# Kernel optimization log

Measured on AMD Instinct MI355X. Metric: run time of the kernel, lower is better.

## Reference

```python
import jax, jax.numpy as jnp
import numpy as np

HEAD = 2

def setup_inputs() -> dict:
    key = jax.random.key(0)
    ks = jax.random.split(key, 12)
    B, C, H, W = 4, 512, 64, 64
    IC = 256
    N = H * W
    s = 0.02
    return {
        "x": jax.random.normal(ks[0], (B, C, H, W), jnp.float32),
        "output_attn": jax.random.normal(ks[1], (B, C, H, W), jnp.float32),
        "mlp_w": jax.random.normal(ks[2], (N, N), jnp.float32) * s,
        "mlp_b": jax.random.normal(ks[3], (N,), jnp.float32) * s,
        "g_w": jax.random.normal(ks[4], (IC, C), jnp.float32) * s,
        "g_b": jax.random.normal(ks[5], (IC,), jnp.float32) * s,
        "theta_w": jax.random.normal(ks[6], (IC, C), jnp.float32) * s,
        "theta_b": jax.random.normal(ks[7], (IC,), jnp.float32) * s,
        "phi_w": jax.random.normal(ks[8], (IC, C), jnp.float32) * s,
        "phi_b": jax.random.normal(ks[9], (IC,), jnp.float32) * s,
        "out_w": jax.random.normal(ks[10], (C, IC), jnp.float32) * s,
        "out_b": jax.random.normal(ks[11], (C,), jnp.float32) * s,
    }

def _conv1x1(feat, w, b):
    # feat: [B, Cin, N], w: [Cout, Cin], b: [Cout] -> [B, Cout, N]
    return jnp.einsum('bcn,oc->bon', feat, w) + b[None, :, None]

def reference(x, output_attn, mlp_w, mlp_b, g_w, g_b, theta_w, theta_b,
              phi_w, phi_b, out_w, out_b):
    B, C, H, W = x.shape
    N = H * W
    IC = g_w.shape[0]
    d = IC // HEAD  # per-head dim

    xf = x.reshape(B, C, N)
    # head-MLP remix: only hd==HEAD slice is non-empty (integer-division bug in source)
    xf = xf + (jnp.einsum('bcn,mn->bcm', xf, mlp_w) + mlp_b)

    g = _conv1x1(xf, g_w, g_b)                       # [B, IC, N]
    g = g.reshape(B * HEAD, d, N).transpose(0, 2, 1)  # [BH, N, d]

    oa = output_attn.reshape(B, C, N)
    th = _conv1x1(oa, theta_w, theta_b).reshape(B * HEAD, d, N).transpose(0, 2, 1)  # [BH, N, d]
    ph = _conv1x1(xf, phi_w, phi_b).reshape(B * HEAD, d, N)                          # [BH, d, N]

    scale = 1.0 / (d ** 0.5)
    attn = jax.nn.softmax(jnp.einsum('bnd,bdm->bnm', th, ph) * scale, axis=-1)  # [BH, N, N]
    y = jnp.einsum('bnm,bmd->bnd', attn, g)           # [BH, N, d]
    y = y.reshape(B, HEAD, N, d).transpose(0, 2, 1, 3).reshape(B, N, IC)
    y = y.transpose(0, 2, 1)                          # [B, IC, N]

    out = output_attn + _conv1x1(y, out_w, out_b).reshape(B, C, H, W)
    return out
```

## Files before the change

kernel.cpp:

```cpp
#include <hip/hip_runtime.h>

typedef unsigned short us;
typedef us s8v __attribute__((ext_vector_type(8)));
typedef us s4v __attribute__((ext_vector_type(4)));
typedef float f4v __attribute__((ext_vector_type(4)));
typedef float f16v __attribute__((ext_vector_type(16)));
typedef __bf16 b2v __attribute__((ext_vector_type(2)));

static __device__ __forceinline__ us f2b(float f) {
  return __builtin_bit_cast(us, (__bf16)f);
}
static __device__ __forceinline__ unsigned f2b2(float lo, float hi) {
  b2v v = {(__bf16)lo, (__bf16)hi};
  return __builtin_bit_cast(unsigned, v);
}
static __device__ __forceinline__ float b2f(us s) {
  unsigned u = ((unsigned)s) << 16;
  return __builtin_bit_cast(float, u);
}

#define GLDS(src, dst)                                                        \
  __builtin_amdgcn_global_load_lds(                                           \
      (const __attribute__((address_space(1))) unsigned int*)(src),           \
      (__attribute__((address_space(3))) unsigned int*)(dst), 16, 0, 0)

__global__ __launch_bounds__(256) void castk(const float* __restrict__ in,
                                             us* __restrict__ out, int n4) {
  int i = blockIdx.x * 256 + threadIdx.x;
  int stride = gridDim.x * 256;
  for (; i < n4; i += stride) {
    float4 v = ((const float4*)in)[i];
    s4v s = {f2b(v.x), f2b(v.y), f2b(v.z), f2b(v.w)};
    ((s4v*)out)[i] = s;
  }
}

__global__ __launch_bounds__(256) void wcast4(const float* __restrict__ s0, us* __restrict__ o0,
                                              const float* __restrict__ s1, us* __restrict__ o1,
                                              const float* __restrict__ s2, us* __restrict__ o2,
                                              const float* __restrict__ s3, us* __restrict__ o3) {
  const float* s; us* o;
  int y = blockIdx.y;
  if (y == 0) { s = s0; o = o0; }
  else if (y == 1) { s = s1; o = o1; }
  else if (y == 2) { s = s2; o = o2; }
  else { s = s3; o = o3; }
  int i = blockIdx.x * 256 + threadIdx.x;
  for (; i < 32768; i += 8192) {
    float4 v = ((const float4*)s)[i];
    s4v r = {f2b(v.x), f2b(v.y), f2b(v.z), f2b(v.w)};
    ((s4v*)o)[i] = r;
  }
}

__global__ __launch_bounds__(256) void tcast(const float* __restrict__ in,
                                             us* __restrict__ out, int R, int C,
                                             us* __restrict__ out2) {
  __shared__ float t[64][65];
  const int tid = threadIdx.x;
  const long r0 = (long)blockIdx.y * 64, c0 = (long)blockIdx.x * 64;
#pragma unroll
  for (int j = 0; j < 4; ++j) {
    int idx = j * 256 + tid;
    int row = idx >> 4, c4 = (idx & 15) * 4;
    float4 v = *(const float4*)(in + (r0 + row) * C + c0 + c4);
    t[row][c4] = v.x; t[row][c4 + 1] = v.y; t[row][c4 + 2] = v.z; t[row][c4 + 3] = v.w;
    if (out2) {
      s4v s = {f2b(v.x), f2b(v.y), f2b(v.z), f2b(v.w)};
      *(s4v*)(out2 + (r0 + row) * C + c0 + c4) = s;
    }
  }
  __syncthreads();
#pragma unroll
  for (int j = 0; j < 4; ++j) {
    int idx = j * 256 + tid;
    int orow = idx >> 4, r4 = (idx & 15) * 4;
    s4v s = {f2b(t[r4][orow]), f2b(t[r4 + 1][orow]), f2b(t[r4 + 2][orow]), f2b(t[r4 + 3][orow])};
    *(s4v*)(out + (c0 + orow) * R + r0 + r4) = s;
  }
}

#define SW(row, kb) ((row) * 128 + ((kb) ^ (((row) & 7) << 4)))

template <int EPI, int AF32, int BF32, int SWZ>
__global__ __launch_bounds__(256) void gemm_nt(
    const void* __restrict__ Av, const void* __restrict__ Bv,
    int lda, int ldb, int K, long aZ, long bZ,
    const float* __restrict__ bias,
    const us* __restrict__ addb16,
    const float* __restrict__ addf32,
    us* __restrict__ outb16,
    float* __restrict__ outf32) {
  __shared__ __align__(16) us lA2[2][128 * 64];
  __shared__ __align__(16) us lB2[2][128 * 64];
  const int tid = threadIdx.x, l = tid & 63;
  const int lr = l & 15, lg = l >> 4;
  const int w = tid >> 6, wr = w >> 1, wc = w & 1;
  int bm, bn;
  if constexpr (SWZ) {
    int flat = blockIdx.y * gridDim.x + blockIdx.x;
    int re = (flat & 7) * ((gridDim.x * gridDim.y) >> 3) + (flat >> 3);
    bm = re % gridDim.x; bn = re / gridDim.x;
  } else { bm = blockIdx.x; bn = blockIdx.y; }
  const int z = blockIdx.z;
  const f4v zero = {0.f, 0.f, 0.f, 0.f};
  f4v acc[4][4];
#pragma unroll
  for (int i = 0; i < 4; ++i)
#pragma unroll
    for (int j = 0; j < 4; ++j) acc[i][j] = zero;

  int rS[4], cS[4];
#pragma unroll
  for (int j = 0; j < 4; ++j) {
    int byte = j * 4096 + tid * 16;
    rS[j] = byte >> 7;
    cS[j] = (byte & 127) ^ ((rS[j] & 7) << 4);
  }
  const char* Ab = (const char*)Av + ((long)z * aZ + (long)bm * 128 * lda) * 2;
  const char* Bb = (const char*)Bv + ((long)z * bZ + (long)bn * 128 * ldb) * 2;

  auto stage = [&](int bufi, int k0) {
    char* lab = (char*)lA2[bufi];
    char* lbb = (char*)lB2[bufi];
#pragma unroll
    for (int j = 0; j < 4; ++j) {
      if constexpr (AF32) {
        int byte = j * 4096 + tid * 16;
        int row = byte >> 7, kb = byte & 127;
        const float* af = (const float*)Av + (long)z * aZ + (long)(bm * 128 + row) * lda + k0 + (kb >> 1);
        float4 v0 = *(const float4*)af, v1 = *(const float4*)(af + 4);
        s8v va = {f2b(v0.x), f2b(v0.y), f2b(v0.z), f2b(v0.w), f2b(v1.x), f2b(v1.y), f2b(v1.z), f2b(v1.w)};
        *(s8v*)(lab + SW(row, kb)) = va;
      } else {
        GLDS(Ab + (long)rS[j] * lda * 2 + k0 * 2 + cS[j], lab + j * 4096 + w * 1024);
      }
      if constexpr (BF32) {
        int byte = j * 4096 + tid * 16;
        int row = byte >> 7, kb = byte & 127;
        const float* bf_ = (const float*)Bv + (long)z * bZ + (long)(bn * 128 + row) * ldb + k0 + (kb >> 1);
        float4 v0 = *(const float4*)bf_, v1 = *(const float4*)(bf_ + 4);
        s8v vb = {f2b(v0.x), f2b(v0.y), f2b(v0.z), f2b(v0.w), f2b(v1.x), f2b(v1.y), f2b(v1.z), f2b(v1.w)};
        *(s8v*)(lbb + SW(row, kb)) = vb;
      } else {
        GLDS(Bb + (long)rS[j] * ldb * 2 + k0 * 2 + cS[j], lbb + j * 4096 + w * 1024);
      }
    }
  };

  stage(0, 0);
  for (int k0 = 0; k0 < K; k0 += 64) {
    const int cur = (k0 >> 6) & 1;
    __syncthreads();
    if (k0 + 64 < K) stage(cur ^ 1, k0 + 64);
    const char* lab = (const char*)lA2[cur];
    const char* lbb = (const char*)lB2[cur];
#pragma unroll
    for (int ks = 0; ks < 2; ++ks) {
      s8v af[4], bf[4];
      const int kb = ks * 64 + lg * 16;
#pragma unroll
      for (int mi = 0; mi < 4; ++mi) {
        int row = wr * 64 + mi * 16 + lr;
        af[mi] = *(const s8v*)(lab + SW(row, kb));
      }
#pragma unroll
      for (int ni = 0; ni < 4; ++ni) {
        int row = wc * 64 + ni * 16 + lr;
        bf[ni] = *(const s8v*)(lbb + SW(row, kb));
      }
#pragma unroll
      for (int mi = 0; mi < 4; ++mi)
#pragma unroll
        for (int ni = 0; ni < 4; ++ni)
          acc[mi][ni] = __builtin_amdgcn_mfma_f32_16x16x32_bf16(af[mi], bf[ni], acc[mi][ni], 0, 0, 0);
    }
  }

#pragma unroll
  for (int mi = 0; mi < 4; ++mi) {
#pragma unroll
    for (int ni = 0; ni < 4; ++ni) {
#pragma unroll
      for (int r = 0; r < 4; ++r) {
        int row = bm * 128 + wr * 64 + mi * 16 + lg * 4 + r;
        int col = bn * 128 + wc * 64 + ni * 16 + lr;
        float v = acc[mi][ni][r];
        if constexpr (EPI == 0) {
          long idx = (long)row * 2048 + col;
          outb16[idx] = f2b(v + b2f(addb16[idx]) + bias[row]);
        } else if constexpr (EPI == 1) {
          long idx = ((long)(z * 2 + (col >> 7)) * 4096 + row) * 128 + (col & 127);
          outb16[idx] = f2b(v + bias[col]);
        } else if constexpr (EPI == 2) {
          long idx = ((long)(z * 256 + row)) * 4096 + col;
          outb16[idx] = f2b(v + bias[row]);
        } else {
          long idx = ((long)(z * 512 + row)) * 4096 + col;
          outf32[idx] = v + bias[row] + addf32[idx];
        }
      }
    }
  }
}

__global__ __launch_bounds__(256, 2) void attn_k(const us* __restrict__ th,
                                                 const us* __restrict__ pht,
                                                 const us* __restrict__ g,
                                                 us* __restrict__ pY,
                                                 float2* __restrict__ pml) {
  __shared__ __align__(16) us ph2[2][64 * 128];
  __shared__ __align__(16) us g2[2][128 * 64];
  const int tid = threadIdx.x, l = tid & 63, w = tid >> 6;
  const int l31 = l & 31, h = l >> 5;
  const int swz = (l & 7) << 4;
  const int flat = blockIdx.y * 32 + blockIdx.x;
  const int bh = flat & 7, rest = flat >> 3;
  const int half = rest & 1, qb = rest >> 1;
  const int b = bh >> 1, head = bh & 1;
  const int m00 = half * 2048;
  const float C1 = 0.12751802f;
  const f16v zero16 = {0.f};

  const char* phsrc = (const char*)(pht + (long)bh * 4096 * 128);
  const char* gsrc = (const char*)(g + (long)(b * 256 + head * 128) * 4096);

  int koff[4], voff[4];
#pragma unroll
  for (int j = 0; j < 4; ++j) {
    int d = j * 4096 + tid * 16;
    koff[j] = d ^ (((d >> 8) & 7) << 4);
    int rowg = d >> 7, kbg = d & 127;
    voff[j] = rowg * 8192 + (kbg ^ ((rowg & 7) << 4));
  }

  s8v qf[8];
  {
    const us* thp = th + ((long)bh * 4096 + qb * 128 + w * 32 + l31) * 128 + h * 8;
#pragma unroll
    for (int ks = 0; ks < 8; ++ks) qf[ks] = *(const s8v*)(thp + ks * 16);
  }

  f16v acc0 = zero16, acc1 = zero16, acc2 = zero16, acc3 = zero16;
  float m_run = -1e30f, l_run = 0.f;

  auto stage = [&](int bufi, int m0) {
    char* dk = (char*)ph2[bufi] + w * 1024;
    char* dv = (char*)g2[bufi] + w * 1024;
    const char* sk = phsrc + (long)m0 * 256;
    const char* sv = gsrc + (long)m0 * 2;
#pragma unroll
    for (int j = 0; j < 4; ++j) {
      GLDS(sk + koff[j], dk + j * 4096);
      GLDS(sv + voff[j], dv + j * 4096);
    }
  };

  stage(0, m00);
  __syncthreads();

  for (int t = 0; t < 32; ++t) {
    const int cur = t & 1;
    stage(cur ^ 1, m00 + ((t + 1) & 31) * 64);
    const char* phb = (const char*)ph2[cur];
    const char* gb = (const char*)g2[cur];

    f16v sA[2] = {zero16, zero16};
    __builtin_amdgcn_s_setprio(1);
#pragma unroll
    for (int ks = 0; ks < 8; ++ks) {
#pragma unroll
      for (int mt = 0; mt < 2; ++mt) {
        s8v kf = *(const s8v*)(phb + (mt * 32 + l31) * 256 + (((ks * 32) + h * 16) ^ swz));
        sA[mt] = __builtin_amdgcn_mfma_f32_32x32x16_bf16(kf, qf[ks], sA[mt], 0, 0, 0);
      }
    }
    __builtin_amdgcn_s_setprio(0);

    float mx = sA[0][0];
#pragma unroll
    for (int r = 1; r < 16; ++r) mx = fmaxf(mx, sA[0][r]);
#pragma unroll
    for (int r = 0; r < 16; ++r) mx = fmaxf(mx, sA[1][r]);
    mx = fmaxf(mx, __shfl_xor(mx, 32, 64));

    if (__any(mx > m_run + 60.0f)) {
      float mn = fmaxf(m_run, mx);
      float corr = __builtin_amdgcn_exp2f((m_run - mn) * C1);
      m_run = mn;
      l_run *= corr;
#pragma unroll
      for (int r = 0; r < 16; ++r) {
        acc0[r] *= corr; acc1[r] *= corr; acc2[r] *= corr; acc3[r] *= corr;
      }
    }

    const float nm = -m_run * C1;
    float sum = 0.f;
    s8v bfrag[4];
#pragma unroll
    for (int mt = 0; mt < 2; ++mt) {
#pragma unroll
      for (int k1 = 0; k1 < 2; ++k1) {
        const int base = k1 * 8;
        float p0 = __builtin_amdgcn_exp2f(__builtin_fmaf(sA[mt][base + 0], C1, nm));
        float p1 = __builtin_amdgcn_exp2f(__builtin_fmaf(sA[mt][base + 1], C1, nm));
        float p2 = __builtin_amdgcn_exp2f(__builtin_fmaf(sA[mt][base + 2], C1, nm));
        float p3 = __builtin_amdgcn_exp2f(__builtin_fmaf(sA[mt][base + 3], C1, nm));
        float p4 = __builtin_amdgcn_exp2f(__builtin_fmaf(sA[mt][base + 4], C1, nm));
        float p5 = __builtin_amdgcn_exp2f(__builtin_fmaf(sA[mt][base + 5], C1, nm));
        float p6 = __builtin_amdgcn_exp2f(__builtin_fmaf(sA[mt][base + 6], C1, nm));
        float p7 = __builtin_amdgcn_exp2f(__builtin_fmaf(sA[mt][base + 7], C1, nm));
        sum += ((p0 + p1) + (p2 + p3)) + ((p4 + p5) + (p6 + p7));
        unsigned E0 = f2b2(p0, p1), E1 = f2b2(p2, p3);
        unsigned O0 = f2b2(p4, p5), O1 = f2b2(p6, p7);
        asm("v_permlane32_swap_b32 %0, %1" : "+v"(E0), "+v"(O0));
        asm("v_permlane32_swap_b32 %0, %1" : "+v"(E1), "+v"(O1));
        uint4 u = {E0, E1, O0, O1};
        bfrag[mt * 2 + k1] = __builtin_bit_cast(s8v, u);
      }
    }
    sum += __shfl_xor(sum, 32, 64);
    l_run += sum;

    __builtin_amdgcn_s_setprio(1);
#pragma unroll
    for (int ks2 = 0; ks2 < 4; ++ks2) {
      const int kb = ((ks2 * 32) + h * 16) ^ swz;
      s8v v0 = *(const s8v*)(gb + (l31) * 128 + kb);
      s8v v1 = *(const s8v*)(gb + (32 + l31) * 128 + kb);
      s8v v2 = *(const s8v*)(gb + (64 + l31) * 128 + kb);
      s8v v3 = *(const s8v*)(gb + (96 + l31) * 128 + kb);
      acc0 = __builtin_amdgcn_mfma_f32_32x32x16_bf16(v0, bfrag[ks2], acc0, 0, 0, 0);
      acc1 = __builtin_amdgcn_mfma_f32_32x32x16_bf16(v1, bfrag[ks2], acc1, 0, 0, 0);
      acc2 = __builtin_amdgcn_mfma_f32_32x32x16_bf16(v2, bfrag[ks2], acc2, 0, 0, 0);
      acc3 = __builtin_amdgcn_mfma_f32_32x32x16_bf16(v3, bfrag[ks2], acc3, 0, 0, 0);
    }
    __builtin_amdgcn_s_setprio(0);

    __syncthreads();
  }

  const long gq = (long)bh * 4096 + qb * 128 + w * 32 + l31;
  if (h == 0) pml[gq * 2 + half] = make_float2(m_run, l_run);
  us* py = pY + (gq * 2 + half) * 128;
#pragma unroll
  for (int gi = 0; gi < 4; ++gi) {
    int r0 = gi * 4;
    {
      uint2 u = {f2b2(acc0[r0], acc0[r0 + 1]), f2b2(acc0[r0 + 2], acc0[r0 + 3])};
      *(uint2*)(py + gi * 8 + 4 * h) = u;
    }
    {
      uint2 u = {f2b2(acc1[r0], acc1[r0 + 1]), f2b2(acc1[r0 + 2], acc1[r0 + 3])};
      *(uint2*)(py + 32 + gi * 8 + 4 * h) = u;
    }
    {
      uint2 u = {f2b2(acc2[r0], acc2[r0 + 1]), f2b2(acc2[r0 + 2], acc2[r0 + 3])};
      *(uint2*)(py + 64 + gi * 8 + 4 * h) = u;
    }
    {
      uint2 u = {f2b2(acc3[r0], acc3[r0 + 1]), f2b2(acc3[r0 + 2], acc3[r0 + 3])};
      *(uint2*)(py + 96 + gi * 8 + 4 * h) = u;
    }
  }
}

__global__ __launch_bounds__(256) void mergek(const us* __restrict__ pY,
                                              const float2* __restrict__ pml,
                                              us* __restrict__ yt) {
  const float C1 = 0.12751802f;
  int idx = blockIdx.x * 256 + threadIdx.x;
  int gq = idx >> 4, dd8 = (idx & 15) * 8;
  float2 A = pml[gq * 2 + 0], B = pml[gq * 2 + 1];
  float M = fmaxf(A.x, B.x);
  float e0 = __builtin_amdgcn_exp2f((A.x - M) * C1);
  float e1 = __builtin_amdgcn_exp2f((B.x - M) * C1);
  float inv = 1.0f / (A.y * e0 + B.y * e1);
  e0 *= inv; e1 *= inv;
  s8v Y0 = *(const s8v*)(pY + ((long)gq * 2 + 0) * 128 + dd8);
  s8v Y1 = *(const s8v*)(pY + ((long)gq * 2 + 1) * 128 + dd8);
  s8v o;
#pragma unroll
  for (int i = 0; i < 8; ++i) o[i] = f2b(e0 * b2f(Y0[i]) + e1 * b2f(Y1[i]));
  int bh = gq >> 12, q = gq & 4095, b = bh >> 1, head = bh & 1;
  *(s8v*)(yt + ((long)b * 4096 + q) * 256 + head * 128 + dd8) = o;
}

extern "C" void kernel_launch(void* const* d_in, const int* in_sizes, int n_in,
                              void* d_out, int out_size, void* d_ws, size_t ws_size,
                              hipStream_t stream) {
  (void)in_sizes; (void)n_in; (void)out_size;
  const float* x       = (const float*)d_in[0];
  const float* oa      = (const float*)d_in[1];
  const float* mlp_w   = (const float*)d_in[2];
  const float* mlp_b   = (const float*)d_in[3];
  const float* g_w     = (const float*)d_in[4];
  const float* g_b     = (const float*)d_in[5];
  const float* theta_w = (const float*)d_in[6];
  const float* theta_b = (const float*)d_in[7];
  const float* phi_w   = (const float*)d_in[8];
  const float* phi_b   = (const float*)d_in[9];
  const float* out_w   = (const float*)d_in[10];
  const float* out_b   = (const float*)d_in[11];
  float* out = (float*)d_out;
  char* ws = (char*)d_ws;

  us* xf_t   = (us*)(ws + 0L);
  us* pY     = (us*)(ws + 0L);
  us* oat    = (us*)(ws + 16777216L);
  float2* pml = (float2*)(ws + 16777216L);
  us* xt     = (us*)(ws + 33554432L);
  us* g_ws   = (us*)(ws + 33554432L);
  us* th_ws  = (us*)(ws + 41943040L);
  us* xc     = (us*)(ws + 50331648L);
  us* ph_ws  = (us*)(ws + 50331648L);
  us* yt     = (us*)(ws + 58720256L);
  us* g_wb   = (us*)(ws + 67108864L);
  us* th_wb  = (us*)(ws + 67371008L);
  us* ph_wb  = (us*)(ws + 67633152L);
  us* out_wb = (us*)(ws + 67895296L);
  us* mlp_wb = (us*)(ws + 68157440L);
  const bool big = ws_size >= 101711872ULL;

  wcast4<<<dim3(32, 4), dim3(256), 0, stream>>>(g_w, g_wb, theta_w, th_wb,
                                                phi_w, ph_wb, out_w, out_wb);
  tcast<<<dim3(64, 32), dim3(256), 0, stream>>>(x, xt, 2048, 4096, xc);
  tcast<<<dim3(64, 32), dim3(256), 0, stream>>>(oa, oat, 2048, 4096, nullptr);

  if (big) {
    castk<<<dim3(1024), dim3(256), 0, stream>>>(mlp_w, mlp_wb, 4194304);
    gemm_nt<0, 0, 0, 1><<<dim3(32, 16, 1), dim3(256), 0, stream>>>(
        mlp_wb, xc, 4096, 4096, 4096, 0, 0, mlp_b, xt, nullptr, xf_t, nullptr);
  } else {
    gemm_nt<0, 1, 0, 1><<<dim3(32, 16, 1), dim3(256), 0, stream>>>(
        mlp_w, xc, 4096, 4096, 4096, 0, 0, mlp_b, xt, nullptr, xf_t, nullptr);
  }

  gemm_nt<1, 0, 0, 0><<<dim3(32, 2, 4), dim3(256), 0, stream>>>(
      oat, th_wb, 2048, 512, 512, 512, 0, theta_b, nullptr, nullptr, th_ws, nullptr);
  gemm_nt<1, 0, 0, 0><<<dim3(32, 2, 4), dim3(256), 0, stream>>>(
      xf_t, ph_wb, 2048, 512, 512, 512, 0, phi_b, nullptr, nullptr, ph_ws, nullptr);
  gemm_nt<2, 0, 0, 0><<<dim3(2, 32, 4), dim3(256), 0, stream>>>(
      g_wb, xf_t, 512, 2048, 512, 0, 512, g_b, nullptr, nullptr, g_ws, nullptr);

  attn_k<<<dim3(32, 16), dim3(256), 0, stream>>>(th_ws, ph_ws, g_ws, pY, pml);
  mergek<<<dim3(2048), dim3(256), 0, stream>>>(pY, pml, yt);

  gemm_nt<3, 0, 0, 0><<<dim3(4, 32, 4), dim3(256), 0, stream>>>(
      out_wb, yt, 256, 256, 256, 0, 1048576L, out_b, nullptr, oa, nullptr, out);
}
```

Measured before the change: 255.5 us.

## Use triple-buffered half-K tiles with explicit vmcnt waits in gemm and attention

Both the GEMM and attention kernels move from double-buffered 64-wide K tiles to triple-buffered 32-wide tiles, prefetching two stages ahead. A partial s_waitcnt vmcnt(4) plus a raw barrier replaces __syncthreads, so the next tile's loads can stay in flight while the current one is computed. The GEMM drops its LDS swizzle, which may bring back bank conflicts. The attention kernel halves per-iteration work, doubling loop count and barriers, and issues fewer MFMAs between syncs.

```diff
diff --git a/kernel.cpp b/kernel.cpp
--- a/kernel.cpp
+++ b/kernel.cpp
@@ -23,6 +23,13 @@
   __builtin_amdgcn_global_load_lds(                                           \
       (const __attribute__((address_space(1))) unsigned int*)(src),           \
       (__attribute__((address_space(3))) unsigned int*)(dst), 16, 0, 0)
+
+#define WAITBAR_VM4()  do { asm volatile("s_waitcnt vmcnt(4)" ::: "memory");  \
+  __builtin_amdgcn_sched_barrier(0); __builtin_amdgcn_s_barrier(); } while (0)
+#define WAITBAR_VM0()  do { asm volatile("s_waitcnt vmcnt(0)" ::: "memory");  \
+  __builtin_amdgcn_sched_barrier(0); __builtin_amdgcn_s_barrier(); } while (0)
+#define WAITBAR_ALL()  do { asm volatile("s_waitcnt vmcnt(0) lgkmcnt(0)" ::: "memory"); \
+  __builtin_amdgcn_sched_barrier(0); __builtin_amdgcn_s_barrier(); } while (0)
 
 __global__ __launch_bounds__(256) void castk(const float* __restrict__ in,
                                              us* __restrict__ out, int n4) {
@@ -80,8 +87,6 @@
   }
 }
 
-#define SW(row, kb) ((row) * 128 + ((kb) ^ (((row) & 7) << 4)))
-
 template <int EPI, int AF32, int BF32, int SWZ>
 __global__ __launch_bounds__(256) void gemm_nt(
     const void* __restrict__ Av, const void* __restrict__ Bv,
@@ -91,8 +96,8 @@
     const float* __restrict__ addf32,
     us* __restrict__ outb16,
     float* __restrict__ outf32) {
-  __shared__ __align__(16) us lA2[2][128 * 64];
-  __shared__ __align__(16) us lB2[2][128 * 64];
+  __shared__ __align__(16) us lA[3][128 * 32];
+  __shared__ __align__(16) us lB[3][128 * 32];
   const int tid = threadIdx.x, l = tid & 63;
   const int lr = l & 15, lg = l >> 4;
   const int w = tid >> 6, wr = w >> 1, wc = w & 1;
@@ -110,71 +115,60 @@
 #pragma unroll
     for (int j = 0; j < 4; ++j) acc[i][j] = zero;
 
-  int rS[4], cS[4];
-#pragma unroll
-  for (int j = 0; j < 4; ++j) {
-    int byte = j * 4096 + tid * 16;
-    rS[j] = byte >> 7;
-    cS[j] = (byte & 127) ^ ((rS[j] & 7) << 4);
-  }
   const char* Ab = (const char*)Av + ((long)z * aZ + (long)bm * 128 * lda) * 2;
   const char* Bb = (const char*)Bv + ((long)z * bZ + (long)bn * 128 * ldb) * 2;
 
   auto stage = [&](int bufi, int k0) {
-    char* lab = (char*)lA2[bufi];
-    char* lbb = (char*)lB2[bufi];
-#pragma unroll
-    for (int j = 0; j < 4; ++j) {
+#pragma unroll
+    for (int j = 0; j < 2; ++j) {
+      const int d = j * 4096 + tid * 16;
+      const int row = d >> 6, kb = d & 63;
       if constexpr (AF32) {
-        int byte = j * 4096 + tid * 16;
-        int row = byte >> 7, kb = byte & 127;
         const float* af = (const float*)Av + (long)z * aZ + (long)(bm * 128 + row) * lda + k0 + (kb >> 1);
         float4 v0 = *(const float4*)af, v1 = *(const float4*)(af + 4);
         s8v va = {f2b(v0.x), f2b(v0.y), f2b(v0.z), f2b(v0.w), f2b(v1.x), f2b(v1.y), f2b(v1.z), f2b(v1.w)};
-        *(s8v*)(lab + SW(row, kb)) = va;
+        *(s8v*)((char*)lA[bufi] + d) = va;
       } else {
-        GLDS(Ab + (long)rS[j] * lda * 2 + k0 * 2 + cS[j], lab + j * 4096 + w * 1024);
+        GLDS(Ab + (long)row * lda * 2 + k0 * 2 + kb, (char*)lA[bufi] + j * 4096 + w * 1024);
       }
       if constexpr (BF32) {
-        int byte = j * 4096 + tid * 16;
-        int row = byte >> 7, kb = byte & 127;
         const float* bf_ = (const float*)Bv + (long)z * bZ + (long)(bn * 128 + row) * ldb + k0 + (kb >> 1);
         float4 v0 = *(const float4*)bf_, v1 = *(const float4*)(bf_ + 4);
         s8v vb = {f2b(v0.x), f2b(v0.y), f2b(v0.z), f2b(v0.w), f2b(v1.x), f2b(v1.y), f2b(v1.z), f2b(v1.w)};
-        *(s8v*)(lbb + SW(row, kb)) = vb;
+        *(s8v*)((char*)lB[bufi] + d) = vb;
       } else {
-        GLDS(Bb + (long)rS[j] * ldb * 2 + k0 * 2 + cS[j], lbb + j * 4096 + w * 1024);
+        GLDS(Bb + (long)row * ldb * 2 + k0 * 2 + kb, (char*)lB[bufi] + j * 4096 + w * 1024);
       }
     }
   };
 
+  const int NT = K >> 5;
   stage(0, 0);
-  for (int k0 = 0; k0 < K; k0 += 64) {
-    const int cur = (k0 >> 6) & 1;
-    __syncthreads();
-    if (k0 + 64 < K) stage(cur ^ 1, k0 + 64);
-    const char* lab = (const char*)lA2[cur];
-    const char* lbb = (const char*)lB2[cur];
-#pragma unroll
-    for (int ks = 0; ks < 2; ++ks) {
-      s8v af[4], bf[4];
-      const int kb = ks * 64 + lg * 16;
-#pragma unroll
-      for (int mi = 0; mi < 4; ++mi) {
-        int row = wr * 64 + mi * 16 + lr;
-        af[mi] = *(const s8v*)(lab + SW(row, kb));
-      }
-#pragma unroll
-      for (int ni = 0; ni < 4; ++ni) {
-        int row = wc * 64 + ni * 16 + lr;
-        bf[ni] = *(const s8v*)(lbb + SW(row, kb));
-      }
-#pragma unroll
-      for (int mi = 0; mi < 4; ++mi)
-#pragma unroll
-        for (int ni = 0; ni < 4; ++ni)
-          acc[mi][ni] = __builtin_amdgcn_mfma_f32_16x16x32_bf16(af[mi], bf[ni], acc[mi][ni], 0, 0, 0);
-    }
+  stage(1, 32);
+  if constexpr (AF32 || BF32) { WAITBAR_ALL(); } else { WAITBAR_VM4(); }
+
+  for (int t = 0; t < NT; ++t) {
+    const int cur = t % 3;
+    const bool more = (t + 2 < NT);
+    if (more) stage((t + 2) % 3, (t + 2) * 32);
+    const char* lab = (const char*)lA[cur];
+    const char* lbb = (const char*)lB[cur];
+    s8v af[4], bf[4];
+#pragma unroll
+    for (int mi = 0; mi < 4; ++mi)
+      af[mi] = *(const s8v*)(lab + (wr * 64 + mi * 16 + lr) * 64 + lg * 16);
+#pragma unroll
+    for (int ni = 0; ni < 4; ++ni)
+      bf[ni] = *(const s8v*)(lbb + (wc * 64 + ni * 16 + lr) * 64 + lg * 16);
+    __builtin_amdgcn_s_setprio(1);
+#pragma unroll
+    for (int mi = 0; mi < 4; ++mi)
+#pragma unroll
+      for (int ni = 0; ni < 4; ++ni)
+        acc[mi][ni] = __builtin_amdgcn_mfma_f32_16x16x32_bf16(af[mi], bf[ni], acc[mi][ni], 0, 0, 0);
+    __builtin_amdgcn_s_setprio(0);
+    if constexpr (AF32 || BF32) { WAITBAR_ALL(); }
+    else if (more) { WAITBAR_VM4(); } else { WAITBAR_VM0(); }
   }
 
 #pragma unroll
@@ -209,11 +203,10 @@
                                                  const us* __restrict__ g,
                                                  us* __restrict__ pY,
                                                  float2* __restrict__ pml) {
-  __shared__ __align__(16) us ph2[2][64 * 128];
-  __shared__ __align__(16) us g2[2][128 * 64];
+  __shared__ __align__(16) us ph3[3][32 * 128];
+  __shared__ __align__(16) us g3[3][128 * 32];
   const int tid = threadIdx.x, l = tid & 63, w = tid >> 6;
   const int l31 = l & 31, h = l >> 5;
-  const int swz = (l & 7) << 4;
   const int flat = blockIdx.y * 32 + blockIdx.x;
   const int bh = flat & 7, rest = flat >> 3;
   const int half = rest & 1, qb = rest >> 1;
@@ -225,15 +218,6 @@
   const char* phsrc = (const char*)(pht + (long)bh * 4096 * 128);
   const char* gsrc = (const char*)(g + (long)(b * 256 + head * 128) * 4096);
 
-  int koff[4], voff[4];
-#pragma unroll
-  for (int j = 0; j < 4; ++j) {
-    int d = j * 4096 + tid * 16;
-    koff[j] = d ^ (((d >> 8) & 7) << 4);
-    int rowg = d >> 7, kbg = d & 127;
-    voff[j] = rowg * 8192 + (kbg ^ ((rowg & 7) << 4));
-  }
-
   s8v qf[8];
   {
     const us* thp = th + ((long)bh * 4096 + qb * 128 + w * 32 + l31) * 128 + h * 8;
@@ -245,43 +229,39 @@
   float m_run = -1e30f, l_run = 0.f;
 
   auto stage = [&](int bufi, int m0) {
-    char* dk = (char*)ph2[bufi] + w * 1024;
-    char* dv = (char*)g2[bufi] + w * 1024;
-    const char* sk = phsrc + (long)m0 * 256;
-    const char* sv = gsrc + (long)m0 * 2;
-#pragma unroll
-    for (int j = 0; j < 4; ++j) {
-      GLDS(sk + koff[j], dk + j * 4096);
-      GLDS(sv + voff[j], dv + j * 4096);
+#pragma unroll
+    for (int j = 0; j < 2; ++j) {
+      const int d = j * 4096 + tid * 16;
+      const int rk = d >> 8, kk = (d & 255) ^ ((rk & 7) << 4);
+      GLDS(phsrc + (long)(m0 + rk) * 256 + kk, (char*)ph3[bufi] + j * 4096 + w * 1024);
+      const int rv = d >> 6, kv = (d & 63) ^ ((rv & 3) << 4);
+      GLDS(gsrc + (long)rv * 8192 + m0 * 2 + kv, (char*)g3[bufi] + j * 4096 + w * 1024);
     }
   };
 
   stage(0, m00);
-  __syncthreads();
-
-  for (int t = 0; t < 32; ++t) {
-    const int cur = t & 1;
-    stage(cur ^ 1, m00 + ((t + 1) & 31) * 64);
-    const char* phb = (const char*)ph2[cur];
-    const char* gb = (const char*)g2[cur];
-
-    f16v sA[2] = {zero16, zero16};
+  stage(1, m00 + 32);
+  WAITBAR_VM4();
+
+  for (int t = 0; t < 64; ++t) {
+    const int cur = t % 3;
+    const bool more = (t + 2 < 64);
+    if (more) stage((t + 2) % 3, m00 + (t + 2) * 32);
+    const char* phb = (const char*)ph3[cur];
+    const char* gb = (const char*)g3[cur];
+
+    f16v sA = zero16;
     __builtin_amdgcn_s_setprio(1);
 #pragma unroll
     for (int ks = 0; ks < 8; ++ks) {
-#pragma unroll
-      for (int mt = 0; mt < 2; ++mt) {
-        s8v kf = *(const s8v*)(phb + (mt * 32 + l31) * 256 + (((ks * 32) + h * 16) ^ swz));
-        sA[mt] = __builtin_amdgcn_mfma_f32_32x32x16_bf16(kf, qf[ks], sA[mt], 0, 0, 0);
-      }
+      s8v kf = *(const s8v*)(phb + l31 * 256 + (((ks * 32) + h * 16) ^ ((l31 & 7) << 4)));
+      sA = __builtin_amdgcn_mfma_f32_32x32x16_bf16(kf, qf[ks], sA, 0, 0, 0);
     }
     __builtin_amdgcn_s_setprio(0);
 
-    float mx = sA[0][0];
-#pragma unroll
-    for (int r = 1; r < 16; ++r) mx = fmaxf(mx, sA[0][r]);
-#pragma unroll
-    for (int r = 0; r < 16; ++r) mx = fmaxf(mx, sA[1][r]);
+    float mx = sA[0];
+#pragma unroll
+    for (int r = 1; r < 16; ++r) mx = fmaxf(mx, sA[r]);
     mx = fmaxf(mx, __shfl_xor(mx, 32, 64));
 
     if (__any(mx > m_run + 60.0f)) {
@@ -297,40 +277,37 @@
 
     const float nm = -m_run * C1;
     float sum = 0.f;
-    s8v bfrag[4];
-#pragma unroll
-    for (int mt = 0; mt < 2; ++mt) {
-#pragma unroll
-      for (int k1 = 0; k1 < 2; ++k1) {
-        const int base = k1 * 8;
-        float p0 = __builtin_amdgcn_exp2f(__builtin_fmaf(sA[mt][base + 0], C1, nm));
-        float p1 = __builtin_amdgcn_exp2f(__builtin_fmaf(sA[mt][base + 1], C1, nm));
-        float p2 = __builtin_amdgcn_exp2f(__builtin_fmaf(sA[mt][base + 2], C1, nm));
-        float p3 = __builtin_amdgcn_exp2f(__builtin_fmaf(sA[mt][base + 3], C1, nm));
-        float p4 = __builtin_amdgcn_exp2f(__builtin_fmaf(sA[mt][base + 4], C1, nm));
-        float p5 = __builtin_amdgcn_exp2f(__builtin_fmaf(sA[mt][base + 5], C1, nm));
-        float p6 = __builtin_amdgcn_exp2f(__builtin_fmaf(sA[mt][base + 6], C1, nm));
-        float p7 = __builtin_amdgcn_exp2f(__builtin_fmaf(sA[mt][base + 7], C1, nm));
-        sum += ((p0 + p1) + (p2 + p3)) + ((p4 + p5) + (p6 + p7));
-        unsigned E0 = f2b2(p0, p1), E1 = f2b2(p2, p3);
-        unsigned O0 = f2b2(p4, p5), O1 = f2b2(p6, p7);
-        asm("v_permlane32_swap_b32 %0, %1" : "+v"(E0), "+v"(O0));
-        asm("v_permlane32_swap_b32 %0, %1" : "+v"(E1), "+v"(O1));
-        uint4 u = {E0, E1, O0, O1};
-        bfrag[mt * 2 + k1] = __builtin_bit_cast(s8v, u);
-      }
+    s8v bfrag[2];
+#pragma unroll
+    for (int k1 = 0; k1 < 2; ++k1) {
+      const int base = k1 * 8;
+      float p0 = __builtin_amdgcn_exp2f(__builtin_fmaf(sA[base + 0], C1, nm));
+      float p1 = __builtin_amdgcn_exp2f(__builtin_fmaf(sA[base + 1], C1, nm));
+      float p2 = __builtin_amdgcn_exp2f(__builtin_fmaf(sA[base + 2], C1, nm));
+      float p3 = __builtin_amdgcn_exp2f(__builtin_fmaf(sA[base + 3], C1, nm));
+      float p4 = __builtin_amdgcn_exp2f(__builtin_fmaf(sA[base + 4], C1, nm));
+      float p5 = __builtin_amdgcn_exp2f(__builtin_fmaf(sA[base + 5], C1, nm));
+      float p6 = __builtin_amdgcn_exp2f(__builtin_fmaf(sA[base + 6], C1, nm));
+      float p7 = __builtin_amdgcn_exp2f(__builtin_fmaf(sA[base + 7], C1, nm));
+      sum += ((p0 + p1) + (p2 + p3)) + ((p4 + p5) + (p6 + p7));
+      unsigned E0 = f2b2(p0, p1), E1 = f2b2(p2, p3);
+      unsigned O0 = f2b2(p4, p5), O1 = f2b2(p6, p7);
+      asm("v_permlane32_swap_b32 %0, %1" : "+v"(E0), "+v"(O0));
+      asm("v_permlane32_swap_b32 %0, %1" : "+v"(E1), "+v"(O1));
+      uint4 u = {E0, E1, O0, O1};
+      bfrag[k1] = __builtin_bit_cast(s8v, u);
     }
     sum += __shfl_xor(sum, 32, 64);
     l_run += sum;
 
     __builtin_amdgcn_s_setprio(1);
 #pragma unroll
-    for (int ks2 = 0; ks2 < 4; ++ks2) {
-      const int kb = ((ks2 * 32) + h * 16) ^ swz;
-      s8v v0 = *(const s8v*)(gb + (l31) * 128 + kb);
-      s8v v1 = *(const s8v*)(gb + (32 + l31) * 128 + kb);
-      s8v v2 = *(const s8v*)(gb + (64 + l31) * 128 + kb);
-      s8v v3 = *(const s8v*)(gb + (96 + l31) * 128 + kb);
+    for (int ks2 = 0; ks2 < 2; ++ks2) {
+      const int kb = ks2 * 32 + h * 16;
+      s8v v0 = *(const s8v*)(gb + (l31) * 64 + (kb ^ ((l31 & 3) << 4)));
+      s8v v1 = *(const s8v*)(gb + (32 + l31) * 64 + (kb ^ ((l31 & 3) << 4)));
+      s8v v2 = *(const s8v*)(gb + (64 + l31) * 64 + (kb ^ ((l31 & 3) << 4)));
+      s8v v3 = *(const s8v*)(gb + (96 + l31) * 64 + (kb ^ ((l31 & 3) << 4)));
       acc0 = __builtin_amdgcn_mfma_f32_32x32x16_bf16(v0, bfrag[ks2], acc0, 0, 0, 0);
       acc1 = __builtin_amdgcn_mfma_f32_32x32x16_bf16(v1, bfrag[ks2], acc1, 0, 0, 0);
       acc2 = __builtin_amdgcn_mfma_f32_32x32x16_bf16(v2, bfrag[ks2], acc2, 0, 0, 0);
@@ -338,7 +315,7 @@
     }
     __builtin_amdgcn_s_setprio(0);
 
-    __syncthreads();
+    if (more) { WAITBAR_VM4(); } else { WAITBAR_VM0(); }
   }
 
   const long gq = (long)bh * 4096 + qb * 128 + w * 32 + l31;
```

New measurement: 302.0 us. +18.2%, slower.
